# Performance work log

Measured on AMD Instinct MI355X. Metric: run time of the kernel, lower is better.

## Reference

```python
import jax, jax.numpy as jnp
import numpy as np

NUM_FRAMES = 36
NUM_QUERIES = 36000            # num_out = 1000
NUM_TGT = 256                  # flat targets = NUM_TGT * NUM_FRAMES = 9216
NUM_CLASSES = 81
COST_CLASS = 1.0
COST_BBOX = 1.0
COST_GIOU = 1.0


def box_cxcywh_to_xyxy(b):
    cx, cy, w, h = b[..., 0], b[..., 1], b[..., 2], b[..., 3]
    return jnp.stack([cx - 0.5 * w, cy - 0.5 * h, cx + 0.5 * w, cy + 0.5 * h], axis=-1)


def multi_giou(a, b):
    # elementwise (broadcasted) generalized IoU over last-dim xyxy boxes
    lt = jnp.maximum(a[..., :2], b[..., :2])
    rb = jnp.minimum(a[..., 2:], b[..., 2:])
    wh = jnp.clip(rb - lt, 0.0)
    inter = wh[..., 0] * wh[..., 1]
    area_a = (a[..., 2] - a[..., 0]) * (a[..., 3] - a[..., 1])
    area_b = (b[..., 2] - b[..., 0]) * (b[..., 3] - b[..., 1])
    union = area_a + area_b - inter
    iou = inter / union
    lt_c = jnp.minimum(a[..., :2], b[..., :2])
    rb_c = jnp.maximum(a[..., 2:], b[..., 2:])
    wh_c = jnp.clip(rb_c - lt_c, 0.0)
    area_c = wh_c[..., 0] * wh_c[..., 1]
    return iou - (area_c - union) / area_c


def setup_inputs() -> dict:
    key = jax.random.key(0)
    k1, k2, k3, k4 = jax.random.split(key, 4)
    pred_logits = jax.random.normal(k1, (NUM_QUERIES, NUM_CLASSES), dtype=jnp.float32)
    pred_boxes = jax.random.uniform(k2, (NUM_QUERIES, 4), dtype=jnp.float32,
                                    minval=0.05, maxval=0.95)
    tgt_bbox = jax.random.uniform(k3, (NUM_TGT * NUM_FRAMES, 4), dtype=jnp.float32,
                                  minval=0.05, maxval=0.95)
    tgt_ids = jax.random.randint(k4, (NUM_TGT * NUM_FRAMES,), 0, NUM_CLASSES)
    return {
        "pred_logits": pred_logits,
        "pred_boxes": pred_boxes,
        "tgt_bbox": tgt_bbox,
        "tgt_ids": tgt_ids,
        "num_frames": NUM_FRAMES,
    }


def reference(pred_logits, pred_boxes, tgt_bbox, tgt_ids, num_frames):
    Q, C = pred_logits.shape
    F = num_frames
    O = Q // F                      # num_out (queries per frame / tracks)
    T = tgt_ids.shape[0] // F       # num targets (tracks)

    out_prob = jax.nn.softmax(pred_logits, axis=-1)
    # [F, O, C] -> [O, F, C]
    out_prob_split = jnp.transpose(out_prob.reshape(F, O, C), (1, 0, 2))
    # gather over (frame, class) pairs: frame_index repeats 0..F-1 per target
    frame_index = jnp.tile(jnp.arange(F), T)          # [T*F]
    class_cost = -out_prob_split[:, frame_index, tgt_ids]      # [O, T*F]
    class_cost = class_cost.reshape(O, T, F).mean(axis=-1)     # [O, T]

    # [O, 1, F, 4] vs [1, T, F, 4]
    out_bbox_split = jnp.transpose(pred_boxes.reshape(F, O, 4), (1, 0, 2))[:, None]
    tgt_bbox_split = tgt_bbox.reshape(T, F, 4)[None]
    bbox_cost = jnp.abs(out_bbox_split - tgt_bbox_split).mean(axis=(-1, -2))  # [O, T]

    giou = multi_giou(box_cxcywh_to_xyxy(out_bbox_split),
                      box_cxcywh_to_xyxy(tgt_bbox_split))       # [O, T, F]
    iou_cost = -giou.mean(axis=-1)                              # [O, T]

    cost = COST_CLASS * class_cost + COST_BBOX * bbox_cost + COST_GIOU * iou_cost
    return cost
```

## Files before the change

### kernel.cpp

```cpp
#include <hip/hip_runtime.h>
#include <hip/hip_bf16.h>

#define NF 36
#define NO 1000
#define NT 256
#define NC 81

#define WS_BYTES (NF * NT * 16 + (NF / 4) * NT * 4)

__global__ __launch_bounds__(256) void matcher_prep_kernel(
    const float* __restrict__ tboxes,
    const int*   __restrict__ tids,
    float4* __restrict__ tb_x,
    uchar4* __restrict__ pk)
{
    const int i = blockIdx.x * 256 + threadIdx.x;
    if (i < NF * NT) {
        const int f = i / NT, t = i - f * NT;
        const float4 b = ((const float4*)tboxes)[t * NF + f];
        float4 x;
        x.x = b.x - 0.5f * b.z;  x.y = b.y - 0.5f * b.w;
        x.z = b.x + 0.5f * b.z;  x.w = b.y + 0.5f * b.w;
        tb_x[i] = x;
    }
    if (i < (NF / 4) * NT) {
        const int fb4 = i / NT, t = i - fb4 * NT;
        const int4 v = *(const int4*)(tids + t * NF + fb4 * 4);
        uchar4 u;
        u.x = (unsigned char)v.x;  u.y = (unsigned char)v.y;
        u.z = (unsigned char)v.z;  u.w = (unsigned char)v.w;
        pk[i] = u;
    }
}

__global__ __launch_bounds__(256, 4) void matcher_main_kernel(
    const float* __restrict__ logits,
    const float* __restrict__ pboxes,
    const float4* __restrict__ tb_x,
    const uchar4* __restrict__ pk,
    float* __restrict__ out)
{
    const int o    = blockIdx.x;
    const int tid  = threadIdx.x;
    const int wave = tid >> 6;
    const int lane = tid & 63;

    __shared__ float  prob[NF * NC];
    __shared__ float4 pbx[NF];
    __shared__ float  pbarea[NF];

    if (tid < NF) {
        const float4 pc = ((const float4*)pboxes)[tid * NO + o];
        float4 x;
        x.x = pc.x - 0.5f * pc.z;  x.y = pc.y - 0.5f * pc.w;
        x.z = pc.x + 0.5f * pc.z;  x.w = pc.y + 0.5f * pc.w;
        pbx[tid] = x;
        pbarea[tid] = pc.z * pc.w;
    }

    for (int f = wave; f < NF; f += 4) {
        const float* row = logits + (size_t)(f * NO + o) * NC;
        float e1 = (lane      < NC) ? __expf(row[lane])      : 0.0f;
        float e2 = (lane + 64 < NC) ? __expf(row[lane + 64]) : 0.0f;
        float s = e1 + e2;
        #pragma unroll
        for (int m = 32; m; m >>= 1) s += __shfl_xor(s, m);
        const float inv = __builtin_amdgcn_rcpf(s);
        if (lane      < NC) prob[f * NC + lane]      = e1 * inv;
        if (lane + 64 < NC) prob[f * NC + lane + 64] = e2 * inv;
    }
    __syncthreads();

    const int t = tid;
    float acc_cls = 0.0f, acc_l1 = 0.0f, acc_giou = 0.0f;

    #pragma unroll 2
    for (int fb = 0; fb < NF; fb += 4) {
        const uchar4 c4 = pk[(fb >> 2) * NT + t];
        float4 tx[4];
        #pragma unroll
        for (int j = 0; j < 4; ++j) tx[j] = tb_x[(fb + j) * NT + t];
        const int cls[4] = {c4.x, c4.y, c4.z, c4.w};

        #pragma unroll
        for (int j = 0; j < 4; ++j) {
            const int f = fb + j;
            const float4 tv = tx[j];
            const float4 pb = pbx[f];

            acc_cls += prob[f * NC + cls[j]];

            const float dx0 = pb.x - tv.x, dy0 = pb.y - tv.y;
            const float dx1 = pb.z - tv.z, dy1 = pb.w - tv.w;
            acc_l1 += 0.5f * (fabsf(dx0 + dx1) + fabsf(dy0 + dy1))
                    + fabsf(dx1 - dx0) + fabsf(dy1 - dy0);

            const float ltx = fmaxf(pb.x, tv.x), lty = fmaxf(pb.y, tv.y);
            const float rbx = fminf(pb.z, tv.z), rby = fminf(pb.w, tv.w);
            const float inter = fmaxf(rbx - ltx, 0.0f) * fmaxf(rby - lty, 0.0f);

            const float area_b = (tv.z - tv.x) * (tv.w - tv.y);
            const float uni = pbarea[f] + area_b - inter;

            const float cx0 = fminf(pb.x, tv.x), cy0 = fminf(pb.y, tv.y);
            const float cx1 = fmaxf(pb.z, tv.z), cy1 = fmaxf(pb.w, tv.w);
            const float area_c = (cx1 - cx0) * (cy1 - cy0);

            acc_giou += inter * __builtin_amdgcn_rcpf(uni)
                      - (area_c - uni) * __builtin_amdgcn_rcpf(area_c);
        }
    }

    const float inv_f  = 1.0f / (float)NF;
    const float inv_4f = 1.0f / (float)(4 * NF);
    out[(size_t)o * NT + t] = -acc_cls * inv_f + acc_l1 * inv_4f - acc_giou * inv_f;
}

__global__ __launch_bounds__(256) void matcher_fallback_kernel(
    const float* __restrict__ logits, const float* __restrict__ pboxes,
    const float* __restrict__ tboxes, const int* __restrict__ tids,
    float* __restrict__ out)
{
    const int o = blockIdx.x, tid = threadIdx.x;
    const int wave = tid >> 6, lane = tid & 63;
    __shared__ float prob[NF * NC];
    __shared__ float pb[NF][4];
    for (int f = wave; f < NF; f += 4) {
        const float* row = logits + (size_t)(f * NO + o) * NC;
        float e1 = (lane < NC) ? __expf(row[lane]) : 0.0f;
        float e2 = (lane + 64 < NC) ? __expf(row[lane + 64]) : 0.0f;
        float s = e1 + e2;
        #pragma unroll
        for (int m = 32; m; m >>= 1) s += __shfl_xor(s, m);
        const float inv = 1.0f / s;
        if (lane < NC)      prob[f * NC + lane]      = e1 * inv;
        if (lane + 64 < NC) prob[f * NC + lane + 64] = e2 * inv;
    }
    if (tid < NF * 4) {
        const int f = tid >> 2, k = tid & 3;
        pb[f][k] = pboxes[(size_t)(f * NO + o) * 4 + k];
    }
    __syncthreads();
    const int t = tid;
    const float4* tb4 = (const float4*)tboxes;
    float acc_cls = 0.0f, acc_l1 = 0.0f, acc_giou = 0.0f;
    for (int f = 0; f < NF; ++f) {
        const int cls = tids[t * NF + f];
        const float4 tb = tb4[t * NF + f];
        acc_cls += prob[f * NC + cls];
        const float pcx = pb[f][0], pcy = pb[f][1], pw = pb[f][2], ph = pb[f][3];
        acc_l1 += fabsf(pcx - tb.x) + fabsf(pcy - tb.y) + fabsf(pw - tb.z) + fabsf(ph - tb.w);
        const float ax0 = pcx - 0.5f * pw, ay0 = pcy - 0.5f * ph;
        const float ax1 = pcx + 0.5f * pw, ay1 = pcy + 0.5f * ph;
        const float bx0 = tb.x - 0.5f * tb.z, by0 = tb.y - 0.5f * tb.w;
        const float bx1 = tb.x + 0.5f * tb.z, by1 = tb.y + 0.5f * tb.w;
        const float ltx = fmaxf(ax0, bx0), lty = fmaxf(ay0, by0);
        const float rbx = fminf(ax1, bx1), rby = fminf(ay1, by1);
        const float inter = fmaxf(rbx - ltx, 0.0f) * fmaxf(rby - lty, 0.0f);
        const float uni = (ax1 - ax0) * (ay1 - ay0) + (bx1 - bx0) * (by1 - by0) - inter;
        const float cx0 = fminf(ax0, bx0), cy0 = fminf(ay0, by0);
        const float cx1 = fmaxf(ax1, bx1), cy1 = fmaxf(ay1, by1);
        const float area_c = fmaxf(cx1 - cx0, 0.0f) * fmaxf(cy1 - cy0, 0.0f);
        acc_giou += inter / uni - (area_c - uni) / area_c;
    }
    out[(size_t)o * NT + t] = (-acc_cls - acc_giou) * (1.0f / NF) + acc_l1 * (1.0f / (4 * NF));
}

extern "C" void kernel_launch(void* const* d_in, const int* in_sizes, int n_in,
                              void* d_out, int out_size, void* d_ws, size_t ws_size,
                              hipStream_t stream) {
    const float* pred_logits = (const float*)d_in[0];
    const float* pred_boxes  = (const float*)d_in[1];
    const float* tgt_bbox    = (const float*)d_in[2];
    const int*   tgt_ids     = (const int*)d_in[3];
    float* out = (float*)d_out;

    if (ws_size >= (size_t)WS_BYTES) {
        float4* tb_x = (float4*)d_ws;
        uchar4* pk   = (uchar4*)(tb_x + NF * NT);
        matcher_prep_kernel<<<(NF * NT + 255) / 256, 256, 0, stream>>>(
            tgt_bbox, tgt_ids, tb_x, pk);
        matcher_main_kernel<<<NO, 256, 0, stream>>>(
            pred_logits, pred_boxes, tb_x, pk, out);
    } else {
        matcher_fallback_kernel<<<NO, 256, 0, stream>>>(
            pred_logits, pred_boxes, tgt_bbox, tgt_ids, out);
    }
}
```

Measured before the change: 90.11 us.

## Move softmax into prep kernel and store probabilities transposed in workspace

The per-row softmax over logits moves out of the main kernel into the prep kernel, which now runs one wave per row across 9000 extra blocks. Probabilities are written to workspace in a per-query contiguous layout [O][F][C]. The main kernel then just copies one contiguous 11.6KB chunk into shared memory with float4 loads instead of gathering 36 strided rows and doing exp and reductions. This adds a full workspace round-trip of the probability tensor and a larger prep launch, in exchange for more parallel softmax and coalesced loads in the main kernel.

```diff
diff --git a/kernel.cpp b/kernel.cpp
--- a/kernel.cpp
+++ b/kernel.cpp
@@ -6,49 +6,78 @@
 #define NT 256
 #define NC 81
 
-#define WS_BYTES (NF * NT * 16 + (NF / 4) * NT * 4)
+#define NROWS (NF * NO)
+#define SM_BLOCKS (NROWS / 4)
+#define TP_BLOCKS ((NF * NT + 255) / 256)
+
+#define WS_BYTES (NF * NT * 16 + NROWS * NC * 4 + (NF / 4) * NT * 4)
 
 __global__ __launch_bounds__(256) void matcher_prep_kernel(
+    const float* __restrict__ logits,
     const float* __restrict__ tboxes,
     const int*   __restrict__ tids,
+    float*  __restrict__ prob_ws,
     float4* __restrict__ tb_x,
     uchar4* __restrict__ pk)
 {
-    const int i = blockIdx.x * 256 + threadIdx.x;
-    if (i < NF * NT) {
-        const int f = i / NT, t = i - f * NT;
-        const float4 b = ((const float4*)tboxes)[t * NF + f];
-        float4 x;
-        x.x = b.x - 0.5f * b.z;  x.y = b.y - 0.5f * b.w;
-        x.z = b.x + 0.5f * b.z;  x.w = b.y + 0.5f * b.w;
-        tb_x[i] = x;
-    }
-    if (i < (NF / 4) * NT) {
-        const int fb4 = i / NT, t = i - fb4 * NT;
-        const int4 v = *(const int4*)(tids + t * NF + fb4 * 4);
-        uchar4 u;
-        u.x = (unsigned char)v.x;  u.y = (unsigned char)v.y;
-        u.z = (unsigned char)v.z;  u.w = (unsigned char)v.w;
-        pk[i] = u;
+    const int b = blockIdx.x;
+    if (b < SM_BLOCKS) {
+        const int wave = threadIdx.x >> 6;
+        const int lane = threadIdx.x & 63;
+        const int r = b * 4 + wave;
+        const int f = r / NO;
+        const int o = r - f * NO;
+        const float* row = logits + (size_t)r * NC;
+        float e1 = (lane      < NC) ? __expf(row[lane])      : 0.0f;
+        float e2 = (lane + 64 < NC) ? __expf(row[lane + 64]) : 0.0f;
+        float s = e1 + e2;
+        #pragma unroll
+        for (int m = 32; m; m >>= 1) s += __shfl_xor(s, m);
+        const float inv = __builtin_amdgcn_rcpf(s);
+        float* dst = prob_ws + (size_t)o * (NF * NC) + f * NC;
+        if (lane      < NC) dst[lane]      = e1 * inv;
+        if (lane + 64 < NC) dst[lane + 64] = e2 * inv;
+    } else {
+        const int i = (b - SM_BLOCKS) * 256 + threadIdx.x;
+        if (i < NF * NT) {
+            const int f = i / NT, t = i - f * NT;
+            const float4 bb = ((const float4*)tboxes)[t * NF + f];
+            float4 x;
+            x.x = bb.x - 0.5f * bb.z;  x.y = bb.y - 0.5f * bb.w;
+            x.z = bb.x + 0.5f * bb.z;  x.w = bb.y + 0.5f * bb.w;
+            tb_x[i] = x;
+        }
+        if (i < (NF / 4) * NT) {
+            const int fb4 = i / NT, t = i - fb4 * NT;
+            const int4 v = *(const int4*)(tids + t * NF + fb4 * 4);
+            uchar4 u;
+            u.x = (unsigned char)v.x;  u.y = (unsigned char)v.y;
+            u.z = (unsigned char)v.z;  u.w = (unsigned char)v.w;
+            pk[i] = u;
+        }
     }
 }
 
 __global__ __launch_bounds__(256, 4) void matcher_main_kernel(
-    const float* __restrict__ logits,
     const float* __restrict__ pboxes,
+    const float* __restrict__ prob_ws,
     const float4* __restrict__ tb_x,
     const uchar4* __restrict__ pk,
     float* __restrict__ out)
 {
-    const int o    = blockIdx.x;
-    const int tid  = threadIdx.x;
-    const int wave = tid >> 6;
-    const int lane = tid & 63;
+    const int o   = blockIdx.x;
+    const int tid = threadIdx.x;
 
     __shared__ float  prob[NF * NC];
     __shared__ float4 pbx[NF];
     __shared__ float  pbarea[NF];
 
+    {
+        const float4* src = (const float4*)(prob_ws + (size_t)o * (NF * NC));
+        float4* dst = (float4*)prob;
+        #pragma unroll
+        for (int i = tid; i < (NF * NC) / 4; i += 256) dst[i] = src[i];
+    }
     if (tid < NF) {
         const float4 pc = ((const float4*)pboxes)[tid * NO + o];
         float4 x;
@@ -56,18 +85,6 @@
         x.z = pc.x + 0.5f * pc.z;  x.w = pc.y + 0.5f * pc.w;
         pbx[tid] = x;
         pbarea[tid] = pc.z * pc.w;
-    }
-
-    for (int f = wave; f < NF; f += 4) {
-        const float* row = logits + (size_t)(f * NO + o) * NC;
-        float e1 = (lane      < NC) ? __expf(row[lane])      : 0.0f;
-        float e2 = (lane + 64 < NC) ? __expf(row[lane + 64]) : 0.0f;
-        float s = e1 + e2;
-        #pragma unroll
-        for (int m = 32; m; m >>= 1) s += __shfl_xor(s, m);
-        const float inv = __builtin_amdgcn_rcpf(s);
-        if (lane      < NC) prob[f * NC + lane]      = e1 * inv;
-        if (lane + 64 < NC) prob[f * NC + lane + 64] = e2 * inv;
     }
     __syncthreads();
 
@@ -176,12 +193,13 @@
     float* out = (float*)d_out;
 
     if (ws_size >= (size_t)WS_BYTES) {
-        float4* tb_x = (float4*)d_ws;
-        uchar4* pk   = (uchar4*)(tb_x + NF * NT);
-        matcher_prep_kernel<<<(NF * NT + 255) / 256, 256, 0, stream>>>(
-            tgt_bbox, tgt_ids, tb_x, pk);
+        float4* tb_x    = (float4*)d_ws;
+        float*  prob_ws = (float*)(tb_x + NF * NT);
+        uchar4* pk      = (uchar4*)(prob_ws + (size_t)NROWS * NC);
+        matcher_prep_kernel<<<SM_BLOCKS + TP_BLOCKS, 256, 0, stream>>>(
+            pred_logits, tgt_bbox, tgt_ids, prob_ws, tb_x, pk);
         matcher_main_kernel<<<NO, 256, 0, stream>>>(
-            pred_logits, pred_boxes, tb_x, pk, out);
+            pred_boxes, prob_ws, tb_x, pk, out);
     } else {
         matcher_fallback_kernel<<<NO, 256, 0, stream>>>(
             pred_logits, pred_boxes, tgt_bbox, tgt_ids, out);
```

New measurement: 91.40 us. About the same (+1.4%).
